# Kernel optimization log

Measured on AMD Instinct MI355X. Metric: run time of the kernel, lower is better.

Reference implementation:

```python
import jax, jax.numpy as jnp
import numpy as np

B, I, O = 32768, 512, 512
EPS = 1e-5


def setup_inputs() -> dict:
    key = jax.random.key(0)
    ks = jax.random.split(key, 4)
    return {
        "input": jax.random.normal(ks[0], (B, I), dtype=jnp.float32),
        "h": jax.random.normal(ks[1], (B, O), dtype=jnp.float32),
        "c": jax.random.normal(ks[2], (B, O), dtype=jnp.float32),
        "W": jax.random.normal(ks[3], (4 * O, I + O), dtype=jnp.float32) * (1.0 / np.sqrt(I + O)),
        "gamma": jnp.ones((4, O), dtype=jnp.float32),
        "beta": jnp.zeros((4, O), dtype=jnp.float32),
    }


def reference(input, h, c, W, gamma, beta):
    # fused input projection: [B, I+O] @ [I+O, 4O] -> [B, 4, O]
    z = jnp.einsum("bi,gi->bg", jnp.concatenate([input, h], axis=-1), W)
    z = z.reshape(z.shape[0], 4, O)
    # LayerNorm over the trailing [4, O] dims jointly (torch LayerNorm([x, o_size]))
    mean = jnp.mean(z, axis=(-2, -1), keepdims=True)
    var = jnp.var(z, axis=(-2, -1), keepdims=True)
    zn = (z - mean) * jax.lax.rsqrt(var + EPS) * gamma + beta
    f_gate = jax.nn.sigmoid(zn[:, 0])
    i_gate = jax.nn.sigmoid(zn[:, 1])
    o_gate = jax.nn.sigmoid(zn[:, 2])
    # GELU (torch default = exact erf); dropout is identity in eval mode
    h_state = jax.nn.gelu(zn[:, 3], approximate=False)
    cell = f_gate * c + i_gate * h_state
    output = o_gate * cell
    return (output, cell)
```

## Files before the change

### kernel.cpp

```cpp
#include <hip/hip_runtime.h>
#include <hip/hip_bf16.h>
#include <cstdint>
#include <cstddef>

#define BDIM 32768
#define IDIM 512
#define ODIM 512
#define KDIM 1024
#define NDIM 2048

typedef __attribute__((ext_vector_type(8))) __bf16 bf16x8;
typedef __attribute__((ext_vector_type(4))) float f32x4;
typedef __attribute__((ext_vector_type(8))) unsigned short u16x8;

__device__ __forceinline__ unsigned short f2bf(float x) {
  union { float f; uint32_t u; } v; v.f = x;
  uint32_t r = v.u + 0x7FFFu + ((v.u >> 16) & 1u);
  return (unsigned short)(r >> 16);
}

__device__ __forceinline__ float bf2f(unsigned short s) {
  union { uint32_t u; float f; } v; v.u = ((uint32_t)s) << 16;
  return v.f;
}


__global__ __launch_bounds__(256) void pack_a_kernel(const float* __restrict__ in,
                                                     const float* __restrict__ h,
                                                     unsigned short* __restrict__ A) {
  size_t t = (size_t)blockIdx.x * 256 + threadIdx.x;
  size_t e = t * 8;
  size_t b = e >> 10;
  int col = (int)(e & 1023);
  const float* src = (col < IDIM) ? (in + b * IDIM + col)
                                  : (h + b * ODIM + (col - IDIM));
  float4 v0 = ((const float4*)src)[0];
  float4 v1 = ((const float4*)src)[1];
  u16x8 r;
  r[0] = f2bf(v0.x); r[1] = f2bf(v0.y); r[2] = f2bf(v0.z); r[3] = f2bf(v0.w);
  r[4] = f2bf(v1.x); r[5] = f2bf(v1.y); r[6] = f2bf(v1.z); r[7] = f2bf(v1.w);
  *(u16x8*)(A + e) = r;
}

__global__ __launch_bounds__(256) void pack_w_kernel(const float* __restrict__ Wsrc,
                                                     unsigned short* __restrict__ Wb) {
  size_t t = (size_t)blockIdx.x * 256 + threadIdx.x;
  size_t e = t * 8;
  float4 v0 = ((const float4*)(Wsrc + e))[0];
  float4 v1 = ((const float4*)(Wsrc + e))[1];
  u16x8 r;
  r[0] = f2bf(v0.x); r[1] = f2bf(v0.y); r[2] = f2bf(v0.z); r[3] = f2bf(v0.w);
  r[4] = f2bf(v1.x); r[5] = f2bf(v1.y); r[6] = f2bf(v1.z); r[7] = f2bf(v1.w);
  *(u16x8*)(Wb + e) = r;
}


#define BUFSZ 32768

#define BAR() do { asm volatile("" ::: "memory"); __builtin_amdgcn_s_barrier(); asm volatile("" ::: "memory"); } while (0)
#define VMW(n) asm volatile("s_waitcnt vmcnt(" #n ")" ::: "memory")

__device__ __forceinline__ void gll16(const unsigned short* src, char* ldsdst) {
  __builtin_amdgcn_global_load_lds(
      (const __attribute__((address_space(1))) void*)src,
      (__attribute__((address_space(3))) void*)ldsdst, 16, 0, 0);
}

template<int BUF, int VM, bool STG>
__device__ __forceinline__ void ktile(char* smem, char* aR, char* bR,
                                      const unsigned short* pA0, const unsigned short* pA1,
                                      const unsigned short* pB0, const unsigned short* pB1,
                                      int stOff, f32x4 (&acc)[8][4]) {
  constexpr int CB = BUF * BUFSZ;
  constexpr int DB = ((BUF + 3) & 3) * BUFSZ;

  if (VM == 8)      VMW(8);
  else if (VM == 4) VMW(4);
  else              VMW(0);
  BAR();

  bf16x8 af[8], qf[4];
#pragma unroll
  for (int i = 0; i < 8; ++i) af[i] = *(const bf16x8*)(aR + CB + i * 1024);
#pragma unroll
  for (int j = 0; j < 4; ++j) qf[j] = *(const bf16x8*)(bR + CB + j * 1024);
  if (STG) {
    gll16(pA0, smem + DB + stOff);
    gll16(pA1, smem + DB + 8192 + stOff);
    gll16(pB0, smem + DB + 16384 + stOff);
    gll16(pB1, smem + DB + 24576 + stOff);
  }
  __builtin_amdgcn_sched_barrier(0);
  __builtin_amdgcn_s_setprio(1);
#pragma unroll
  for (int i = 0; i < 8; ++i)
#pragma unroll
    for (int j = 0; j < 4; ++j)
      acc[i][j] = __builtin_amdgcn_mfma_f32_16x16x32_bf16(af[i], qf[j], acc[i][j], 0, 0, 0);
  __builtin_amdgcn_s_setprio(0);
}

__global__ __launch_bounds__(512, 2) void gemm_kernel(const unsigned short* __restrict__ A,
                                                      const unsigned short* __restrict__ Bt,
                                                      unsigned short* __restrict__ Cz) {
  extern __shared__ char smem[];
  const int tid = threadIdx.x;
  const int w = tid >> 6;
  const int lane = tid & 63;

  const int bid = blockIdx.x;
  const int swz = (bid & 7) * 128 + (bid >> 3);
  const int m0 = (swz >> 3) * 256;
  const int n0 = (swz & 7) * 256;

  const int wm = (w >> 2) * 128;
  const int wn = (w & 3) * 64;
  const int lrow = lane & 15;
  const int lk = (lane >> 4) * 8;

  char* aR = smem + (w >> 2) * 8192 + lane * 16;
  char* bR = smem + 16384 + (w & 3) * 4096 + lane * 16;
  const int stOff = w * 1024 + lane * 16;

  const unsigned short* pA0 = A  + (size_t)(m0 + w * 16       + lrow) * KDIM + lk;
  const unsigned short* pA1 = A  + (size_t)(m0 + (8 + w) * 16 + lrow) * KDIM + lk;
  const unsigned short* pB0 = Bt + (size_t)(n0 + w * 16       + lrow) * KDIM + lk;
  const unsigned short* pB1 = Bt + (size_t)(n0 + (8 + w) * 16 + lrow) * KDIM + lk;

  f32x4 acc[8][4] = {};

#pragma unroll
  for (int t = 0; t < 3; ++t) {
    gll16(pA0 + t * 32, smem + t * BUFSZ + stOff);
    gll16(pA1 + t * 32, smem + t * BUFSZ + 8192 + stOff);
    gll16(pB0 + t * 32, smem + t * BUFSZ + 16384 + stOff);
    gll16(pB1 + t * 32, smem + t * BUFSZ + 24576 + stOff);
  }
  pA0 += 96; pA1 += 96; pB0 += 96; pB1 += 96;

  for (int tt = 0; tt < 7; ++tt) {
    ktile<0, 8, true>(smem, aR, bR, pA0, pA1, pB0, pB1, stOff, acc);
    pA0 += 32; pA1 += 32; pB0 += 32; pB1 += 32;
    ktile<1, 8, true>(smem, aR, bR, pA0, pA1, pB0, pB1, stOff, acc);
    pA0 += 32; pA1 += 32; pB0 += 32; pB1 += 32;
    ktile<2, 8, true>(smem, aR, bR, pA0, pA1, pB0, pB1, stOff, acc);
    pA0 += 32; pA1 += 32; pB0 += 32; pB1 += 32;
    ktile<3, 8, true>(smem, aR, bR, pA0, pA1, pB0, pB1, stOff, acc);
    pA0 += 32; pA1 += 32; pB0 += 32; pB1 += 32;
  }
  ktile<0, 8, true >(smem, aR, bR, pA0, pA1, pB0, pB1, stOff, acc);
  ktile<1, 8, false>(smem, aR, bR, pA0, pA1, pB0, pB1, stOff, acc);
  ktile<2, 4, false>(smem, aR, bR, pA0, pA1, pB0, pB1, stOff, acc);
  ktile<3, 0, false>(smem, aR, bR, pA0, pA1, pB0, pB1, stOff, acc);

#pragma unroll
  for (int mi = 0; mi < 8; ++mi) {
#pragma unroll
    for (int ni = 0; ni < 4; ++ni) {
#pragma unroll
      for (int r = 0; r < 4; ++r) {
        const int row = m0 + wm + mi * 16 + (lane >> 4) * 4 + r;
        const int col = n0 + wn + ni * 16 + lrow;
        Cz[(size_t)row * NDIM + col] = f2bf(acc[mi][ni][r]);
      }
    }
  }
}


__global__ __launch_bounds__(256) void ln_gate_kernel(const unsigned short* __restrict__ z,
                                                      const float* __restrict__ c,
                                                      const float* __restrict__ gamma,
                                                      const float* __restrict__ beta,
                                                      float* __restrict__ out) {
  __shared__ float rowbuf[4][NDIM];
  const int wave = threadIdx.x >> 6;
  const int lane = threadIdx.x & 63;
  const int row = blockIdx.x * 4 + wave;
  const unsigned short* zr = z + (size_t)row * NDIM;

  float s = 0.f, ss = 0.f;
#pragma unroll
  for (int j = 0; j < 4; ++j) {
    const int chunk = j * 64 + lane;
    u16x8 v = *(const u16x8*)(zr + chunk * 8);
    float f[8];
#pragma unroll
    for (int i2 = 0; i2 < 8; ++i2) {
      f[i2] = bf2f(v[i2]);
      s += f[i2];
      ss += f[i2] * f[i2];
    }
    float4* dst = (float4*)&rowbuf[wave][chunk * 8];
    dst[0] = make_float4(f[0], f[1], f[2], f[3]);
    dst[1] = make_float4(f[4], f[5], f[6], f[7]);
  }
#pragma unroll
  for (int off = 32; off > 0; off >>= 1) {
    s += __shfl_xor(s, off, 64);
    ss += __shfl_xor(ss, off, 64);
  }
  const float mean = s * (1.f / (float)NDIM);
  const float var = ss * (1.f / (float)NDIM) - mean * mean;
  const float inv = rsqrtf(var + 1e-5f);

  float* out_o = out + (size_t)row * ODIM;
  float* out_c = out + (size_t)BDIM * ODIM + (size_t)row * ODIM;
  const float* crow = c + (size_t)row * ODIM;

#pragma unroll
  for (int j = 0; j < 8; ++j) {
    const int o = j * 64 + lane;
    float zn[4];
#pragma unroll
    for (int g = 0; g < 4; ++g) {
      float v = (rowbuf[wave][g * ODIM + o] - mean) * inv;
      zn[g] = v * gamma[g * ODIM + o] + beta[g * ODIM + o];
    }
    const float fg = 1.f / (1.f + expf(-zn[0]));
    const float ig = 1.f / (1.f + expf(-zn[1]));
    const float og = 1.f / (1.f + expf(-zn[2]));
    const float x = zn[3];
    const float hs = 0.5f * x * (1.f + erff(x * 0.70710678118654752f));
    const float cc = fg * crow[o] + ig * hs;
    out_c[o] = cc;
    out_o[o] = og * cc;
  }
}


extern "C" void kernel_launch(void* const* d_in, const int* in_sizes, int n_in,
                              void* d_out, int out_size, void* d_ws, size_t ws_size,
                              hipStream_t stream) {
  const float* input = (const float*)d_in[0];
  const float* h     = (const float*)d_in[1];
  const float* c     = (const float*)d_in[2];
  const float* W     = (const float*)d_in[3];
  const float* gamma = (const float*)d_in[4];
  const float* beta  = (const float*)d_in[5];

  unsigned short* A  = (unsigned short*)d_ws;
  unsigned short* Wb = A + (size_t)BDIM * KDIM;
  unsigned short* z  = Wb + (size_t)NDIM * KDIM;
  float* out = (float*)d_out;

  hipFuncSetAttribute((const void*)gemm_kernel,
                      hipFuncAttributeMaxDynamicSharedMemorySize, 131072);

  pack_a_kernel<<<(BDIM * KDIM / 8) / 256, 256, 0, stream>>>(input, h, A);
  pack_w_kernel<<<(NDIM * KDIM / 8) / 256, 256, 0, stream>>>(W, Wb);
  gemm_kernel<<<dim3((BDIM / 256) * (NDIM / 256)), 512, 131072, stream>>>(A, Wb, z);
  ln_gate_kernel<<<BDIM / 4, 256, 0, stream>>>(z, c, gamma, beta, out);
}
```

Before: 283.9 us.

## Double-buffer LDS fragments in registers and interleave reads with MFMAs

Software-pipelines the GEMM main loop so each k-tile's LDS reads for the next tile run while the MFMAs consume fragments loaded in the previous step. The kernel now keeps two register fragment sets. The restructuring also changes the prefetch distance and the vmcnt waits. A sched_group_barrier sequence is added to hint interleaving of LDS reads, global-to-LDS loads and MFMAs. This is meant to hide LDS read latency behind matrix math, at the cost of extra VGPR pressure that could cause spills or lower occupancy under the 512x2 launch bounds.

```diff
diff --git a/kernel.cpp b/kernel.cpp
--- a/kernel.cpp
+++ b/kernel.cpp
@@ -66,38 +66,41 @@
       (__attribute__((address_space(3))) void*)ldsdst, 16, 0, 0);
 }
 
-template<int BUF, int VM, bool STG>
-__device__ __forceinline__ void ktile(char* smem, char* aR, char* bR,
+template<int NBUF, int VM, bool STG>
+__device__ __forceinline__ void ktile(char* smem, const char* aR, const char* bR,
                                       const unsigned short* pA0, const unsigned short* pA1,
                                       const unsigned short* pB0, const unsigned short* pB1,
-                                      int stOff, f32x4 (&acc)[8][4]) {
-  constexpr int CB = BUF * BUFSZ;
-  constexpr int DB = ((BUF + 3) & 3) * BUFSZ;
-
-  if (VM == 8)      VMW(8);
-  else if (VM == 4) VMW(4);
+                                      int stOff,
+                                      bf16x8 (&na)[8], bf16x8 (&nb)[4],
+                                      const bf16x8 (&ca)[8], const bf16x8 (&cb)[4],
+                                      f32x4 (&acc)[8][4]) {
+  constexpr int NB = NBUF * BUFSZ;
+  constexpr int DB = ((NBUF + 2) & 3) * BUFSZ;
+
+  if (VM == 4)      VMW(4);
   else              VMW(0);
   BAR();
 
-  bf16x8 af[8], qf[4];
-#pragma unroll
-  for (int i = 0; i < 8; ++i) af[i] = *(const bf16x8*)(aR + CB + i * 1024);
-#pragma unroll
-  for (int j = 0; j < 4; ++j) qf[j] = *(const bf16x8*)(bR + CB + j * 1024);
+#pragma unroll
+  for (int i = 0; i < 8; ++i) na[i] = *(const bf16x8*)(aR + NB + i * 1024);
+#pragma unroll
+  for (int j = 0; j < 4; ++j) nb[j] = *(const bf16x8*)(bR + NB + j * 1024);
   if (STG) {
     gll16(pA0, smem + DB + stOff);
     gll16(pA1, smem + DB + 8192 + stOff);
     gll16(pB0, smem + DB + 16384 + stOff);
     gll16(pB1, smem + DB + 24576 + stOff);
   }
-  __builtin_amdgcn_sched_barrier(0);
   __builtin_amdgcn_s_setprio(1);
 #pragma unroll
   for (int i = 0; i < 8; ++i)
 #pragma unroll
     for (int j = 0; j < 4; ++j)
-      acc[i][j] = __builtin_amdgcn_mfma_f32_16x16x32_bf16(af[i], qf[j], acc[i][j], 0, 0, 0);
+      acc[i][j] = __builtin_amdgcn_mfma_f32_16x16x32_bf16(ca[i], cb[j], acc[i][j], 0, 0, 0);
   __builtin_amdgcn_s_setprio(0);
+  __builtin_amdgcn_sched_group_barrier(0x100, 12, 0);
+  if (STG) __builtin_amdgcn_sched_group_barrier(0x20, 4, 0);
+  __builtin_amdgcn_sched_group_barrier(0x8, 32, 0);
 }
 
 __global__ __launch_bounds__(512, 2) void gemm_kernel(const unsigned short* __restrict__ A,
@@ -118,8 +121,8 @@
   const int lrow = lane & 15;
   const int lk = (lane >> 4) * 8;
 
-  char* aR = smem + (w >> 2) * 8192 + lane * 16;
-  char* bR = smem + 16384 + (w & 3) * 4096 + lane * 16;
+  const char* aR = smem + (w >> 2) * 8192 + lane * 16;
+  const char* bR = smem + 16384 + (w & 3) * 4096 + lane * 16;
   const int stOff = w * 1024 + lane * 16;
 
   const unsigned short* pA0 = A  + (size_t)(m0 + w * 16       + lrow) * KDIM + lk;
@@ -128,6 +131,7 @@
   const unsigned short* pB1 = Bt + (size_t)(n0 + (8 + w) * 16 + lrow) * KDIM + lk;
 
   f32x4 acc[8][4] = {};
+  bf16x8 faA[8], faB[4], fbA[8], fbB[4];
 
 #pragma unroll
   for (int t = 0; t < 3; ++t) {
@@ -138,20 +142,33 @@
   }
   pA0 += 96; pA1 += 96; pB0 += 96; pB1 += 96;
 
+  VMW(8);
+  BAR();
+#pragma unroll
+  for (int i = 0; i < 8; ++i) faA[i] = *(const bf16x8*)(aR + i * 1024);
+#pragma unroll
+  for (int j = 0; j < 4; ++j) faB[j] = *(const bf16x8*)(bR + j * 1024);
+
   for (int tt = 0; tt < 7; ++tt) {
-    ktile<0, 8, true>(smem, aR, bR, pA0, pA1, pB0, pB1, stOff, acc);
-    pA0 += 32; pA1 += 32; pB0 += 32; pB1 += 32;
-    ktile<1, 8, true>(smem, aR, bR, pA0, pA1, pB0, pB1, stOff, acc);
-    pA0 += 32; pA1 += 32; pB0 += 32; pB1 += 32;
-    ktile<2, 8, true>(smem, aR, bR, pA0, pA1, pB0, pB1, stOff, acc);
-    pA0 += 32; pA1 += 32; pB0 += 32; pB1 += 32;
-    ktile<3, 8, true>(smem, aR, bR, pA0, pA1, pB0, pB1, stOff, acc);
-    pA0 += 32; pA1 += 32; pB0 += 32; pB1 += 32;
-  }
-  ktile<0, 8, true >(smem, aR, bR, pA0, pA1, pB0, pB1, stOff, acc);
-  ktile<1, 8, false>(smem, aR, bR, pA0, pA1, pB0, pB1, stOff, acc);
-  ktile<2, 4, false>(smem, aR, bR, pA0, pA1, pB0, pB1, stOff, acc);
-  ktile<3, 0, false>(smem, aR, bR, pA0, pA1, pB0, pB1, stOff, acc);
+    ktile<1, 4, true>(smem, aR, bR, pA0, pA1, pB0, pB1, stOff, fbA, fbB, faA, faB, acc);
+    pA0 += 32; pA1 += 32; pB0 += 32; pB1 += 32;
+    ktile<2, 4, true>(smem, aR, bR, pA0, pA1, pB0, pB1, stOff, faA, faB, fbA, fbB, acc);
+    pA0 += 32; pA1 += 32; pB0 += 32; pB1 += 32;
+    ktile<3, 4, true>(smem, aR, bR, pA0, pA1, pB0, pB1, stOff, fbA, fbB, faA, faB, acc);
+    pA0 += 32; pA1 += 32; pB0 += 32; pB1 += 32;
+    ktile<0, 4, true>(smem, aR, bR, pA0, pA1, pB0, pB1, stOff, faA, faB, fbA, fbB, acc);
+    pA0 += 32; pA1 += 32; pB0 += 32; pB1 += 32;
+  }
+  ktile<1, 4, true >(smem, aR, bR, pA0, pA1, pB0, pB1, stOff, fbA, fbB, faA, faB, acc);
+  ktile<2, 4, false>(smem, aR, bR, pA0, pA1, pB0, pB1, stOff, faA, faB, fbA, fbB, acc);
+  ktile<3, 0, false>(smem, aR, bR, pA0, pA1, pB0, pB1, stOff, fbA, fbB, faA, faB, acc);
+  __builtin_amdgcn_s_setprio(1);
+#pragma unroll
+  for (int i = 0; i < 8; ++i)
+#pragma unroll
+    for (int j = 0; j < 4; ++j)
+      acc[i][j] = __builtin_amdgcn_mfma_f32_16x16x32_bf16(fbA[i], fbB[j], acc[i][j], 0, 0, 0);
+  __builtin_amdgcn_s_setprio(0);
 
 #pragma unroll
   for (int mi = 0; mi < 8; ++mi) {
```

Measured after the change: 367.7 us. 29.5% more time.
